# Kernel tuning notes

Measured on AMD Instinct MI355X. Metric: run time of the kernel, lower is better.

## Reference

```python
import jax, jax.numpy as jnp
import numpy as np

BATCH = 32768
HIDDEN = 512
OUT = 2
FUTURE_STEPS = 60


def _lstm_cell(x, h, c, w_ih, w_hh, b_ih, b_hh):
    # PyTorch gate order: i, f, g, o
    g = x @ w_ih.T + h @ w_hh.T + b_ih + b_hh
    i, f, gg, o = jnp.split(g, 4, axis=-1)
    c_new = jax.nn.sigmoid(f) * c + jax.nn.sigmoid(i) * jnp.tanh(gg)
    h_new = jax.nn.sigmoid(o) * jnp.tanh(c_new)
    return h_new, c_new


def setup_inputs() -> dict:
    key = jax.random.key(0)
    ks = jax.random.split(key, 16)
    s = 0.05
    inp = {
        "h": jax.random.normal(ks[0], (BATCH, HIDDEN), jnp.float32),
        "w_init_h": jax.random.normal(ks[1], (HIDDEN, HIDDEN), jnp.float32) * s,
        "b_init_h": jax.random.normal(ks[2], (HIDDEN,), jnp.float32) * s,
        "w_init_c": jax.random.normal(ks[3], (HIDDEN, HIDDEN), jnp.float32) * s,
        "b_init_c": jax.random.normal(ks[4], (HIDDEN,), jnp.float32) * s,
        "w_ih0": jax.random.normal(ks[5], (4 * HIDDEN, OUT), jnp.float32) * s,
        "w_hh0": jax.random.normal(ks[6], (4 * HIDDEN, HIDDEN), jnp.float32) * s,
        "b_ih0": jax.random.normal(ks[7], (4 * HIDDEN,), jnp.float32) * s,
        "b_hh0": jax.random.normal(ks[8], (4 * HIDDEN,), jnp.float32) * s,
        "w_ih1": jax.random.normal(ks[9], (4 * HIDDEN, HIDDEN), jnp.float32) * s,
        "w_hh1": jax.random.normal(ks[10], (4 * HIDDEN, HIDDEN), jnp.float32) * s,
        "b_ih1": jax.random.normal(ks[11], (4 * HIDDEN,), jnp.float32) * s,
        "b_hh1": jax.random.normal(ks[12], (4 * HIDDEN,), jnp.float32) * s,
        "w_out": jax.random.normal(ks[13], (OUT, HIDDEN), jnp.float32) * s,
        "b_out": jax.random.normal(ks[14], (OUT,), jnp.float32) * s,
    }
    return inp


def reference(h, w_init_h, b_init_h, w_init_c, b_init_c,
              w_ih0, w_hh0, b_ih0, b_hh0,
              w_ih1, w_hh1, b_ih1, b_hh1,
              w_out, b_out):
    batch = h.shape[0]
    # same initial (h, c) replicated to both LSTM layers (repeat(2,1,1))
    h0 = h @ w_init_h.T + b_init_h
    c0 = h @ w_init_c.T + b_init_c
    x0 = jnp.zeros((batch, OUT), h.dtype)

    def step(carry, _):
        x, h1, c1, h2, c2 = carry
        h1, c1 = _lstm_cell(x, h1, c1, w_ih0, w_hh0, b_ih0, b_hh0)
        h2, c2 = _lstm_cell(h1, h2, c2, w_ih1, w_hh1, b_ih1, b_hh1)
        pred = h2 @ w_out.T + b_out  # [batch, OUT]
        return (pred, h1, c1, h2, c2), pred

    _, preds = jax.lax.scan(step, (x0, h0, c0, h0, c0), None, length=FUTURE_STEPS)
    return jnp.transpose(preds, (1, 0, 2))  # [batch, future_steps, OUT]
```

## Files before the change

### kernel.cpp

```cpp
#include <hip/hip_runtime.h>

#define HID    512
#define TPB    512
#define NSTEP  60
#define BMI    64

using f32x4 = __attribute__((ext_vector_type(4))) float;
using s16x8 = __attribute__((ext_vector_type(8))) short;

__device__ __forceinline__ unsigned short f2bf(float f) {
    unsigned u = __builtin_bit_cast(unsigned, f);
    u += 0x7fffu + ((u >> 16) & 1u);
    return (unsigned short)(u >> 16);
}
__device__ __forceinline__ float bf2f(unsigned u) {
    return __builtin_bit_cast(float, u << 16);
}
__device__ __forceinline__ float sigm(float x) { return 1.0f / (1.0f + __expf(-x)); }
__device__ __forceinline__ float tanh_(float x) { return 1.0f - 2.0f / (__expf(2.0f * x) + 1.0f); }

__global__ void pack_kernel(const float* __restrict__ w_hh0, const float* __restrict__ w_ih1,
                            const float* __restrict__ w_hh1, const float* __restrict__ w_init_h,
                            const float* __restrict__ w_init_c,
                            const float* __restrict__ b_ih0, const float* __restrict__ b_hh0,
                            const float* __restrict__ b_ih1, const float* __restrict__ b_hh1,
                            unsigned short* __restrict__ PW1, unsigned short* __restrict__ PW2,
                            unsigned short* __restrict__ PI,
                            float* __restrict__ b1, float* __restrict__ b2)
{
    int idx = blockIdx.x * 256 + threadIdx.x;
    if (idx < 1048576) {
        int el = idx & 511, fr = idx >> 9;
        int ks = fr & 15, ct = (fr >> 4) & 7, s = fr >> 7;
        int lane = el >> 3, e = el & 7;
        int cl = ct * 16 + (lane & 15);
        int gcol = (cl >> 5) * 512 + s * 32 + (cl & 31);
        int k = ks * 32 + (lane >> 4) * 8 + e;
        PW1[idx] = f2bf(w_hh0[gcol * 512 + k]);
        return;
    }
    int i2 = idx - 1048576;
    if (i2 >= 0 && i2 < 2097152) {
        int el = i2 & 511, fr = i2 >> 9;
        int ks = fr & 31, ct = (fr >> 5) & 7, s = fr >> 8;
        int lane = el >> 3, e = el & 7;
        int cl = ct * 16 + (lane & 15);
        int gcol = (cl >> 5) * 512 + s * 32 + (cl & 31);
        int kk = (ks & 15) * 32 + (lane >> 4) * 8 + e;
        float v = (ks < 16) ? w_ih1[gcol * 512 + kk] : w_hh1[gcol * 512 + kk];
        PW2[i2] = f2bf(v);
        return;
    }
    int i3 = idx - (1048576 + 2097152);
    if (i3 >= 0 && i3 < 524288) {
        int el = i3 & 511, fr = i3 >> 9;
        int ks = fr & 15, tile = fr >> 4;
        int s = tile >> 5, c = tile & 31;
        int lane = el >> 3, e = el & 7;
        int n = c * 16 + (lane & 15);
        int k = ks * 32 + (lane >> 4) * 8 + e;
        float v = s ? w_init_c[n * 512 + k] : w_init_h[n * 512 + k];
        PI[i3] = f2bf(v);
        return;
    }
    int i4 = idx - (1048576 + 2097152 + 524288);
    if (i4 >= 0 && i4 < 2048) b1[i4] = b_ih0[i4] + b_hh0[i4];
    else if (i4 >= 2048 && i4 < 4096) b2[i4 - 2048] = b_ih1[i4 - 2048] + b_hh1[i4 - 2048];
}

__global__ __launch_bounds__(TPB, 2) void init_kernel(
    const float* __restrict__ hin, const unsigned short* __restrict__ PI,
    const float* __restrict__ b_init_h, const float* __restrict__ b_init_c,
    unsigned short* __restrict__ h1s, unsigned short* __restrict__ h2s,
    unsigned short* __restrict__ c1s, unsigned short* __restrict__ c2s,
    float* __restrict__ xs0, float* __restrict__ xs1)
{
    __shared__ unsigned short bufA[BMI * HID];
    const int tid = threadIdx.x, lane = tid & 63, wave = tid >> 6;
    const int m0 = blockIdx.x * BMI;
    const int l15 = lane & 15, lg = lane >> 4;
    const int swz = (lane & 7) << 4;

    for (int j = 0; j < 16; ++j) {
        int e = tid * 4 + j * 2048;
        int row = e >> 9, col = e & 511;
        float4 v = *(const float4*)(hin + (size_t)(m0 + row) * HID + col);
        ushort4 w;
        w.x = f2bf(v.x); w.y = f2bf(v.y); w.z = f2bf(v.z); w.w = f2bf(v.w);
        int L = (row * 1024 + col * 2) ^ ((row & 7) << 4);
        *(ushort4*)((char*)bufA + L) = w;
    }
    if (tid < 2 * BMI) { xs0[m0 * 2 + tid] = 0.0f; xs1[m0 * 2 + tid] = 0.0f; }
    __syncthreads();

    #pragma unroll 1
    for (int cc = 0; cc < 4; ++cc) {
        int c = wave * 4 + cc;
        int nc = c * 16 + l15;
        f32x4 acc[4][2];
        #pragma unroll
        for (int rt = 0; rt < 4; ++rt)
            #pragma unroll
            for (int s = 0; s < 2; ++s)
                #pragma unroll
                for (int r = 0; r < 4; ++r) acc[rt][s][r] = 0.0f;

        #pragma unroll
        for (int ks = 0; ks < 16; ++ks) {
            s16x8 a[4];
            #pragma unroll
            for (int rt = 0; rt < 4; ++rt) {
                int ao = (rt * 16 + l15) * 1024 + ((ks * 64 + lg * 16) ^ swz);
                a[rt] = *(const s16x8*)((const char*)bufA + ao);
            }
            #pragma unroll
            for (int s = 0; s < 2; ++s) {
                s16x8 b = ((const s16x8*)PI)[((s * 32 + c) * 16 + ks) * 64 + lane];
                #pragma unroll
                for (int rt = 0; rt < 4; ++rt)
                    acc[rt][s] = __builtin_amdgcn_mfma_f32_16x16x32_bf16(a[rt], b, acc[rt][s], 0, 0, 0);
            }
        }
        float bh = b_init_h[nc], bc = b_init_c[nc];
        #pragma unroll
        for (int rt = 0; rt < 4; ++rt)
            #pragma unroll
            for (int r = 0; r < 4; ++r) {
                int m = m0 + rt * 16 + lg * 4 + r;
                float hv = acc[rt][0][r] + bh;
                float cv = acc[rt][1][r] + bc;
                unsigned short hb = f2bf(hv);
                size_t o = (size_t)m * HID + nc;
                h1s[o] = hb; h2s[o] = hb;
                c1s[o] = f2bf(cv); c2s[o] = f2bf(cv);
            }
    }
}

__global__ __launch_bounds__(TPB, 2) void l1_kernel(
    const unsigned short* __restrict__ h1R, unsigned short* __restrict__ h1W,
    unsigned short* __restrict__ c1s,
    const float* __restrict__ xsR, float* __restrict__ xsW,
    float* __restrict__ outp,
    const unsigned short* __restrict__ PW1, const float* __restrict__ b1,
    const float* __restrict__ w_ih0, const float* __restrict__ b_out, int t)
{
    __shared__ __align__(16) unsigned short Ab[32 * HID];
    __shared__ __align__(16) float gl[32 * 128];
    const int tid = threadIdx.x, lane = tid & 63, w = tid >> 6;
    const int b = blockIdx.x;
    const int g = 2 * (b & 7) + (b >> 7);
    const int s = (b >> 3) & 15;
    const int m0 = g * 2048;
    const int l15 = lane & 15, lg = lane >> 4;

    for (int i = tid; i < 2048; i += TPB)
        *(float2*)(xsW + (size_t)(m0 + i) * 2) = make_float2(0.f, 0.f);

    if (t > 0 && s == 0) {
        float a0 = b_out[0], a1 = b_out[1];
        for (int i = tid; i < 2048; i += TPB) {
            float2 v = *(const float2*)(xsR + (size_t)(m0 + i) * 2);
            float* op = outp + (size_t)(m0 + i) * (2 * NSTEP) + (t - 1) * 2;
            op[0] = v.x + a0; op[1] = v.y + a1;
        }
    }

    s16x8 bw[16];
    #pragma unroll
    for (int ks = 0; ks < 16; ++ks)
        bw[ks] = ((const s16x8*)PW1)[((s * 8 + w) * 16 + ks) * 64 + lane];

    const int erow = tid >> 4, ejp = tid & 15;
    float b1v[8], wiA[8], wiB[8];
    #pragma unroll
    for (int q = 0; q < 8; ++q) {
        int dj = q & 1, gq = q >> 1;
        int gcol = gq * 512 + s * 32 + ejp * 2 + dj;
        b1v[q] = b1[gcol];
        wiA[q] = w_ih0[gcol * 2 + 0];
        wiB[q] = w_ih0[gcol * 2 + 1];
    }
    float bo0 = b_out[0], bo1 = b_out[1];

    const char* srcBase = (const char*)h1R + (size_t)m0 * (HID * 2);

    uint4 nv[4];
    #pragma unroll
    for (int p = 0; p < 4; ++p)
        nv[p] = *(const uint4*)(srcBase + p * 8192 + tid * 16);
    #pragma unroll
    for (int p = 0; p < 4; ++p) {
        int off = p * 8192 + tid * 16;
        int row = off >> 10, colb = off & 1023;
        *(uint4*)((char*)Ab + row * 1024 + (colb ^ ((row & 7) << 4))) = nv[p];
    }

    #pragma unroll 1
    for (int ch = 0; ch < 64; ++ch) {
        __syncthreads();

        if (ch < 63) {
            const char* src = srcBase + (size_t)(ch + 1) * 32768;
            #pragma unroll
            for (int p = 0; p < 4; ++p)
                nv[p] = *(const uint4*)(src + p * 8192 + tid * 16);
        }

        f32x4 acc0 = {0.f, 0.f, 0.f, 0.f}, acc1 = {0.f, 0.f, 0.f, 0.f};
        #pragma unroll
        for (int ks = 0; ks < 16; ++ks) {
            int kb = (ks * 64 + lg * 16);
            s16x8 a0 = *(const s16x8*)((const char*)Ab + l15 * 1024 + (kb ^ ((l15 & 7) << 4)));
            s16x8 a1 = *(const s16x8*)((const char*)Ab + (l15 + 16) * 1024 + (kb ^ ((l15 & 7) << 4)));
            acc0 = __builtin_amdgcn_mfma_f32_16x16x32_bf16(a0, bw[ks], acc0, 0, 0, 0);
            acc1 = __builtin_amdgcn_mfma_f32_16x16x32_bf16(a1, bw[ks], acc1, 0, 0, 0);
        }
        {
            int col = w * 16 + l15;
            int base = (col & 31) * 4 + (col >> 5);
            #pragma unroll
            for (int r = 0; r < 4; ++r) {
                gl[(lg * 4 + r) * 128 + base] = acc0[r];
                gl[(16 + lg * 4 + r) * 128 + base] = acc1[r];
            }
        }
        __syncthreads();

        if (ch < 63) {
            #pragma unroll
            for (int p = 0; p < 4; ++p) {
                int off = p * 8192 + tid * 16;
                int row = off >> 10, colb = off & 1023;
                *(uint4*)((char*)Ab + row * 1024 + (colb ^ ((row & 7) << 4))) = nv[p];
            }
        }

        {
            int m = m0 + ch * 32 + erow;
            float x0 = 0.f, x1 = 0.f;
            if (t > 0) {
                float2 xv = *(const float2*)(xsR + (size_t)m * 2);
                x0 = xv.x + bo0; x1 = xv.y + bo1;
            }
            f32x4 ga = *(const f32x4*)(gl + erow * 128 + ejp * 8);
            f32x4 gb = *(const f32x4*)(gl + erow * 128 + ejp * 8 + 4);
            int cix = m * HID + s * 32 + ejp * 2;
            unsigned cp = *(const unsigned*)(c1s + cix);
            float cold0 = bf2f(cp & 0xffffu), cold1 = bf2f(cp >> 16);
            float i0 = sigm(ga[0] + b1v[0] + x0 * wiA[0] + x1 * wiB[0]);
            float f0 = sigm(ga[1] + b1v[2] + x0 * wiA[2] + x1 * wiB[2]);
            float g0 = tanh_(ga[2] + b1v[4] + x0 * wiA[4] + x1 * wiB[4]);
            float o0 = sigm(ga[3] + b1v[6] + x0 * wiA[6] + x1 * wiB[6]);
            float cn0 = f0 * cold0 + i0 * g0;
            float hn0 = o0 * tanh_(cn0);
            float i1 = sigm(gb[0] + b1v[1] + x0 * wiA[1] + x1 * wiB[1]);
            float f1 = sigm(gb[1] + b1v[3] + x0 * wiA[3] + x1 * wiB[3]);
            float g1 = tanh_(gb[2] + b1v[5] + x0 * wiA[5] + x1 * wiB[5]);
            float o1 = sigm(gb[3] + b1v[7] + x0 * wiA[7] + x1 * wiB[7]);
            float cn1 = f1 * cold1 + i1 * g1;
            float hn1 = o1 * tanh_(cn1);
            *(unsigned*)(c1s + cix) = (unsigned)f2bf(cn0) | ((unsigned)f2bf(cn1) << 16);
            *(unsigned*)(h1W + cix) = (unsigned)f2bf(hn0) | ((unsigned)f2bf(hn1) << 16);
        }
    }
}

__global__ __launch_bounds__(TPB, 2) void l2_kernel(
    const unsigned short* __restrict__ h1C, const unsigned short* __restrict__ h2R,
    unsigned short* __restrict__ h2W, unsigned short* __restrict__ c2s,
    float* __restrict__ xsW,
    const unsigned short* __restrict__ PW2, const float* __restrict__ b2,
    const float* __restrict__ w_out)
{
    __shared__ __align__(16) unsigned short Ab[32 * 1024];
    __shared__ __align__(16) float gl[32 * 128];
    const int tid = threadIdx.x, lane = tid & 63, w = tid >> 6;
    const int b = blockIdx.x;
    const int g = 2 * (b & 7) + (b >> 7);
    const int s = (b >> 3) & 15;
    const int m0 = g * 2048;
    const int l15 = lane & 15, lg = lane >> 4;

    s16x8 bw[32];
    #pragma unroll
    for (int ks = 0; ks < 32; ++ks)
        bw[ks] = ((const s16x8*)PW2)[((s * 8 + w) * 32 + ks) * 64 + lane];

    const int erow = tid >> 4, ejp = tid & 15;
    float b2v[8];
    #pragma unroll
    for (int q = 0; q < 8; ++q) {
        int dj = q & 1, gq = q >> 1;
        b2v[q] = b2[gq * 512 + s * 32 + ejp * 2 + dj];
    }
    float woA0 = w_out[s * 32 + ejp * 2], woA1 = w_out[s * 32 + ejp * 2 + 1];
    float woB0 = w_out[512 + s * 32 + ejp * 2], woB1 = w_out[512 + s * 32 + ejp * 2 + 1];

    const char* s1 = (const char*)h1C + (size_t)m0 * 1024;
    const char* s2 = (const char*)h2R + (size_t)m0 * 1024;

    uint4 nv[8];
    #pragma unroll
    for (int p = 0; p < 8; ++p) {
        int off = p * 8192 + tid * 16;
        int row = off >> 11, colb = off & 2047;
        nv[p] = (colb < 1024) ? *(const uint4*)(s1 + row * 1024 + colb)
                              : *(const uint4*)(s2 + row * 1024 + (colb - 1024));
    }
    #pragma unroll
    for (int p = 0; p < 8; ++p) {
        int off = p * 8192 + tid * 16;
        int row = off >> 11, colb = off & 2047;
        *(uint4*)((char*)Ab + row * 2048 + (colb ^ ((row & 7) << 4))) = nv[p];
    }

    #pragma unroll 1
    for (int ch = 0; ch < 64; ++ch) {
        __syncthreads();

        if (ch < 63) {
            #pragma unroll
            for (int p = 0; p < 8; ++p) {
                int off = p * 8192 + tid * 16;
                int row = (ch + 1) * 32 + (off >> 11), colb = off & 2047;
                nv[p] = (colb < 1024) ? *(const uint4*)(s1 + (size_t)row * 1024 + colb)
                                      : *(const uint4*)(s2 + (size_t)row * 1024 + (colb - 1024));
            }
        }

        f32x4 acc0 = {0.f, 0.f, 0.f, 0.f}, acc1 = {0.f, 0.f, 0.f, 0.f};
        #pragma unroll
        for (int ks = 0; ks < 32; ++ks) {
            int kb = (ks * 64 + lg * 16);
            s16x8 a0 = *(const s16x8*)((const char*)Ab + l15 * 2048 + (kb ^ ((l15 & 7) << 4)));
            s16x8 a1 = *(const s16x8*)((const char*)Ab + (l15 + 16) * 2048 + (kb ^ ((l15 & 7) << 4)));
            acc0 = __builtin_amdgcn_mfma_f32_16x16x32_bf16(a0, bw[ks], acc0, 0, 0, 0);
            acc1 = __builtin_amdgcn_mfma_f32_16x16x32_bf16(a1, bw[ks], acc1, 0, 0, 0);
        }
        {
            int col = w * 16 + l15;
            int base = (col & 31) * 4 + (col >> 5);
            #pragma unroll
            for (int r = 0; r < 4; ++r) {
                gl[(lg * 4 + r) * 128 + base] = acc0[r];
                gl[(16 + lg * 4 + r) * 128 + base] = acc1[r];
            }
        }
        __syncthreads();

        if (ch < 63) {
            #pragma unroll
            for (int p = 0; p < 8; ++p) {
                int off = p * 8192 + tid * 16;
                int row = off >> 11, colb = off & 2047;
                *(uint4*)((char*)Ab + row * 2048 + (colb ^ ((row & 7) << 4))) = nv[p];
            }
        }

        {
            int m = m0 + ch * 32 + erow;
            f32x4 ga = *(const f32x4*)(gl + erow * 128 + ejp * 8);
            f32x4 gb = *(const f32x4*)(gl + erow * 128 + ejp * 8 + 4);
            int cix = m * HID + s * 32 + ejp * 2;
            unsigned cp = *(const unsigned*)(c2s + cix);
            float cold0 = bf2f(cp & 0xffffu), cold1 = bf2f(cp >> 16);
            float i0 = sigm(ga[0] + b2v[0]);
            float f0 = sigm(ga[1] + b2v[2]);
            float g0 = tanh_(ga[2] + b2v[4]);
            float o0 = sigm(ga[3] + b2v[6]);
            float cn0 = f0 * cold0 + i0 * g0;
            float hn0 = o0 * tanh_(cn0);
            float i1 = sigm(gb[0] + b2v[1]);
            float f1 = sigm(gb[1] + b2v[3]);
            float g1 = tanh_(gb[2] + b2v[5]);
            float o1 = sigm(gb[3] + b2v[7]);
            float cn1 = f1 * cold1 + i1 * g1;
            float hn1 = o1 * tanh_(cn1);
            *(unsigned*)(c2s + cix) = (unsigned)f2bf(cn0) | ((unsigned)f2bf(cn1) << 16);
            *(unsigned*)(h2W + cix) = (unsigned)f2bf(hn0) | ((unsigned)f2bf(hn1) << 16);
            float p0 = hn0 * woA0 + hn1 * woA1;
            float p1 = hn0 * woB0 + hn1 * woB1;
            #pragma unroll
            for (int d = 1; d < 16; d <<= 1) {
                p0 += __shfl_xor(p0, d, 16);
                p1 += __shfl_xor(p1, d, 16);
            }
            if (ejp == 0) {
                atomicAdd(xsW + (size_t)m * 2, p0);
                atomicAdd(xsW + (size_t)m * 2 + 1, p1);
            }
        }
    }
}

__global__ void tail_kernel(const float* __restrict__ xs0, const float* __restrict__ b_out,
                            float* __restrict__ outp)
{
    int i = blockIdx.x * 256 + threadIdx.x;
    if (i < 65536) {
        int m = i >> 1, j = i & 1;
        outp[(size_t)m * (2 * NSTEP) + (NSTEP - 1) * 2 + j] = xs0[i] + b_out[j];
    }
}

extern "C" void kernel_launch(void* const* d_in, const int* in_sizes, int n_in,
                              void* d_out, int out_size, void* d_ws, size_t ws_size,
                              hipStream_t stream)
{
    (void)in_sizes; (void)n_in; (void)out_size; (void)ws_size;
    const float* h        = (const float*)d_in[0];
    const float* w_init_h = (const float*)d_in[1];
    const float* b_init_h = (const float*)d_in[2];
    const float* w_init_c = (const float*)d_in[3];
    const float* b_init_c = (const float*)d_in[4];
    const float* w_ih0    = (const float*)d_in[5];
    const float* w_hh0    = (const float*)d_in[6];
    const float* b_ih0    = (const float*)d_in[7];
    const float* b_hh0    = (const float*)d_in[8];
    const float* w_ih1    = (const float*)d_in[9];
    const float* w_hh1    = (const float*)d_in[10];
    const float* b_ih1    = (const float*)d_in[11];
    const float* b_hh1    = (const float*)d_in[12];
    const float* w_out    = (const float*)d_in[13];
    const float* b_out    = (const float*)d_in[14];
    float* out = (float*)d_out;

    char* ws = (char*)d_ws;
    unsigned short* h1s[2] = { (unsigned short*)(ws + 0),
                               (unsigned short*)(ws + 33554432) };
    unsigned short* h2s[2] = { (unsigned short*)(ws + 67108864),
                               (unsigned short*)(ws + 100663296) };
    unsigned short* c1s = (unsigned short*)(ws + 134217728);
    unsigned short* c2s = (unsigned short*)(ws + 167772160);
    float* xs[2] = { (float*)(ws + 201326592), (float*)(ws + 201588736) };
    unsigned short* PW1 = (unsigned short*)(ws + 201850880);
    unsigned short* PW2 = (unsigned short*)(ws + 203948032);
    unsigned short* PI  = (unsigned short*)(ws + 208142336);
    float* b1 = (float*)(ws + 209190912);
    float* b2 = (float*)(ws + 209199104);

    pack_kernel<<<14352, 256, 0, stream>>>(w_hh0, w_ih1, w_hh1, w_init_h, w_init_c,
                                           b_ih0, b_hh0, b_ih1, b_hh1, PW1, PW2, PI, b1, b2);
    init_kernel<<<32768 / BMI, TPB, 0, stream>>>(h, PI, b_init_h, b_init_c,
                                                 h1s[1], h2s[1], c1s, c2s, xs[0], xs[1]);
    for (int t = 0; t < NSTEP; ++t) {
        const unsigned short* h1R = h1s[(t + 1) & 1];
        unsigned short* h1W = h1s[t & 1];
        const unsigned short* h2R = h2s[(t + 1) & 1];
        unsigned short* h2W = h2s[t & 1];
        const float* xsR = xs[t & 1];
        float* xsW = xs[(t + 1) & 1];
        l1_kernel<<<256, TPB, 0, stream>>>(h1R, h1W, c1s, xsR, xsW, out, PW1, b1,
                                           w_ih0, b_out, t);
        l2_kernel<<<256, TPB, 0, stream>>>(h1W, h2R, h2W, c2s, xsW, PW2, b2, w_out);
    }
    tail_kernel<<<256, 256, 0, stream>>>(xs[0], b_out, out);
}
```

Before: 39.92 ms.

## Split MFMA work over K across waves and replace output atomics with partial sums

Each wave now computes four 16-column tiles over half (l1) or a quarter (l2) of the K range. Partial gate sums are reduced through shared memory with a permuted layout to avoid bank conflicts. The h tiles are staged in MFMA-fragment order, so reads need no swizzle. The global atomicAdd accumulation of the output projection is replaced by per-slice partial buffers that the next l1 kernel and the tail kernel sum. This aims to cut LDS A-operand traffic per MFMA and remove atomic contention, at the cost of extra shared-memory reductions and barriers.

```diff
diff --git a/kernel.cpp b/kernel.cpp
--- a/kernel.cpp
+++ b/kernel.cpp
@@ -18,6 +18,15 @@
 }
 __device__ __forceinline__ float sigm(float x) { return 1.0f / (1.0f + __expf(-x)); }
 __device__ __forceinline__ float tanh_(float x) { return 1.0f - 2.0f / (__expf(2.0f * x) + 1.0f); }
+
+__device__ __forceinline__ f32x4 deperm(f32x4 q, int lgr) {
+    f32x4 p;
+    if (lgr == 0)      { p[0]=q[0]; p[1]=q[1]; p[2]=q[2]; p[3]=q[3]; }
+    else if (lgr == 1) { p[0]=q[1]; p[1]=q[0]; p[2]=q[3]; p[3]=q[2]; }
+    else if (lgr == 2) { p[0]=q[2]; p[1]=q[3]; p[2]=q[0]; p[3]=q[1]; }
+    else               { p[0]=q[3]; p[1]=q[2]; p[2]=q[1]; p[3]=q[0]; }
+    return p;
+}
 
 __global__ void pack_kernel(const float* __restrict__ w_hh0, const float* __restrict__ w_ih1,
                             const float* __restrict__ w_hh1, const float* __restrict__ w_init_h,
@@ -72,8 +81,7 @@
     const float* __restrict__ hin, const unsigned short* __restrict__ PI,
     const float* __restrict__ b_init_h, const float* __restrict__ b_init_c,
     unsigned short* __restrict__ h1s, unsigned short* __restrict__ h2s,
-    unsigned short* __restrict__ c1s, unsigned short* __restrict__ c2s,
-    float* __restrict__ xs0, float* __restrict__ xs1)
+    unsigned short* __restrict__ c1s, unsigned short* __restrict__ c2s)
 {
     __shared__ unsigned short bufA[BMI * HID];
     const int tid = threadIdx.x, lane = tid & 63, wave = tid >> 6;
@@ -90,7 +98,6 @@
         int L = (row * 1024 + col * 2) ^ ((row & 7) << 4);
         *(ushort4*)((char*)bufA + L) = w;
     }
-    if (tid < 2 * BMI) { xs0[m0 * 2 + tid] = 0.0f; xs1[m0 * 2 + tid] = 0.0f; }
     __syncthreads();
 
     #pragma unroll 1
@@ -139,39 +146,32 @@
 
 __global__ __launch_bounds__(TPB, 2) void l1_kernel(
     const unsigned short* __restrict__ h1R, unsigned short* __restrict__ h1W,
-    unsigned short* __restrict__ c1s,
-    const float* __restrict__ xsR, float* __restrict__ xsW,
-    float* __restrict__ outp,
-    const unsigned short* __restrict__ PW1, const float* __restrict__ b1,
-    const float* __restrict__ w_ih0, const float* __restrict__ b_out, int t)
+    unsigned short* __restrict__ c1s, const float* __restrict__ pp,
+    float* __restrict__ outp, const unsigned short* __restrict__ PW1,
+    const float* __restrict__ b1, const float* __restrict__ w_ih0,
+    const float* __restrict__ b_out, int t)
 {
-    __shared__ __align__(16) unsigned short Ab[32 * HID];
-    __shared__ __align__(16) float gl[32 * 128];
+    __shared__ __align__(16) unsigned short Ab[16384];
+    __shared__ __align__(16) float gl[2][2][2048];
+    __shared__ __align__(16) float xls[5120];
+
     const int tid = threadIdx.x, lane = tid & 63, w = tid >> 6;
     const int b = blockIdx.x;
     const int g = 2 * (b & 7) + (b >> 7);
     const int s = (b >> 3) & 15;
     const int m0 = g * 2048;
     const int l15 = lane & 15, lg = lane >> 4;
-
-    for (int i = tid; i < 2048; i += TPB)
-        *(float2*)(xsW + (size_t)(m0 + i) * 2) = make_float2(0.f, 0.f);
-
-    if (t > 0 && s == 0) {
-        float a0 = b_out[0], a1 = b_out[1];
-        for (int i = tid; i < 2048; i += TPB) {
-            float2 v = *(const float2*)(xsR + (size_t)(m0 + i) * 2);
-            float* op = outp + (size_t)(m0 + i) * (2 * NSTEP) + (t - 1) * 2;
-            op[0] = v.x + a0; op[1] = v.y + a1;
-        }
-    }
-
-    s16x8 bw[16];
-    #pragma unroll
-    for (int ks = 0; ks < 16; ++ks)
-        bw[ks] = ((const s16x8*)PW1)[((s * 8 + w) * 16 + ks) * 64 + lane];
+    const int cg = w & 1, kh = (w >> 1) & 1, rha = w >> 2;
+
+    s16x8 bw[4][8];
+    #pragma unroll
+    for (int j = 0; j < 4; ++j)
+        #pragma unroll
+        for (int ksl = 0; ksl < 8; ++ksl)
+            bw[j][ksl] = ((const s16x8*)PW1)[(((s * 8 + cg * 4 + j) * 16) + kh * 8 + ksl) * 64 + lane];
 
     const int erow = tid >> 4, ejp = tid & 15;
+    const int lgr = w & 3;
     float b1v[8], wiA[8], wiB[8];
     #pragma unroll
     for (int q = 0; q < 8; ++q) {
@@ -183,81 +183,109 @@
     }
     float bo0 = b_out[0], bo1 = b_out[1];
 
-    const char* srcBase = (const char*)h1R + (size_t)m0 * (HID * 2);
+    if (t == 0) {
+        #pragma unroll
+        for (int i = 0; i < 8; ++i) xls[tid * 8 + i] = 0.0f;
+    } else {
+        f32x4 s0 = {0.f,0.f,0.f,0.f}, s1 = {0.f,0.f,0.f,0.f};
+        #pragma unroll 1
+        for (int ss = 0; ss < 16; ++ss) {
+            const float* p = pp + (((size_t)(g * 16 + ss)) << 12) + tid * 8;
+            s0 += *(const f32x4*)p;
+            s1 += *(const f32x4*)(p + 4);
+        }
+        s0[0] += bo0; s0[1] += bo1; s0[2] += bo0; s0[3] += bo1;
+        s1[0] += bo0; s1[1] += bo1; s1[2] += bo0; s1[3] += bo1;
+        *(f32x4*)(xls + tid * 8) = s0;
+        *(f32x4*)(xls + tid * 8 + 4) = s1;
+        if (s == 0) {
+            float* ob = outp + (size_t)(m0 + tid * 4) * (2 * NSTEP) + (t - 1) * 2;
+            *(float2*)(ob)                 = make_float2(s0[0], s0[1]);
+            *(float2*)(ob + 2 * NSTEP)     = make_float2(s0[2], s0[3]);
+            *(float2*)(ob + 4 * NSTEP)     = make_float2(s1[0], s1[1]);
+            *(float2*)(ob + 6 * NSTEP)     = make_float2(s1[2], s1[3]);
+        }
+    }
+
+    const int sl15 = tid & 15, slg = (tid >> 4) & 3, srh = (tid >> 6) & 1, skq = tid >> 7;
+    const int sgrow = srh * 16 + sl15;
+    const int scol  = (tid & 15) * 0;
+    (void)scol;
 
     uint4 nv[4];
     #pragma unroll
+    for (int p = 0; p < 4; ++p) {
+        int ks = p * 4 + skq;
+        nv[p] = *(const uint4*)(h1R + (size_t)(m0 + sgrow) * HID + ks * 32 + slg * 8);
+    }
+    #pragma unroll
     for (int p = 0; p < 4; ++p)
-        nv[p] = *(const uint4*)(srcBase + p * 8192 + tid * 16);
-    #pragma unroll
-    for (int p = 0; p < 4; ++p) {
-        int off = p * 8192 + tid * 16;
-        int row = off >> 10, colb = off & 1023;
-        *(uint4*)((char*)Ab + row * 1024 + (colb ^ ((row & 7) << 4))) = nv[p];
-    }
+        *(uint4*)((char*)Ab + p * 8192 + tid * 16) = nv[p];
 
     #pragma unroll 1
     for (int ch = 0; ch < 64; ++ch) {
         __syncthreads();
 
         if (ch < 63) {
-            const char* src = srcBase + (size_t)(ch + 1) * 32768;
+            #pragma unroll
+            for (int p = 0; p < 4; ++p) {
+                int ks = p * 4 + skq;
+                nv[p] = *(const uint4*)(h1R + (size_t)(m0 + (ch + 1) * 32 + sgrow) * HID + ks * 32 + slg * 8);
+            }
+        }
+
+        f32x4 acc[4];
+        #pragma unroll
+        for (int j = 0; j < 4; ++j) { acc[j][0]=0.f; acc[j][1]=0.f; acc[j][2]=0.f; acc[j][3]=0.f; }
+        #pragma unroll
+        for (int ksl = 0; ksl < 8; ++ksl) {
+            int ks = kh * 8 + ksl;
+            s16x8 a = *(const s16x8*)((const char*)Ab + ks * 2048 + rha * 1024 + lane * 16);
+            #pragma unroll
+            for (int j = 0; j < 4; ++j)
+                acc[j] = __builtin_amdgcn_mfma_f32_16x16x32_bf16(a, bw[j][ksl], acc[j], 0, 0, 0);
+        }
+        #pragma unroll
+        for (int j = 0; j < 4; ++j) {
+            int col = (cg * 4 + j) * 16 + l15;
+            int u = col & 31, gate = col >> 5;
+            float* dst = &gl[kh][u & 1][(u >> 1) * 4 + (gate ^ lg)];
+            #pragma unroll
+            for (int r = 0; r < 4; ++r)
+                dst[(rha * 16 + lg * 4 + r) * 64] = acc[j][r];
+        }
+        __syncthreads();
+
+        if (ch < 63) {
             #pragma unroll
             for (int p = 0; p < 4; ++p)
-                nv[p] = *(const uint4*)(src + p * 8192 + tid * 16);
-        }
-
-        f32x4 acc0 = {0.f, 0.f, 0.f, 0.f}, acc1 = {0.f, 0.f, 0.f, 0.f};
-        #pragma unroll
-        for (int ks = 0; ks < 16; ++ks) {
-            int kb = (ks * 64 + lg * 16);
-            s16x8 a0 = *(const s16x8*)((const char*)Ab + l15 * 1024 + (kb ^ ((l15 & 7) << 4)));
-            s16x8 a1 = *(const s16x8*)((const char*)Ab + (l15 + 16) * 1024 + (kb ^ ((l15 & 7) << 4)));
-            acc0 = __builtin_amdgcn_mfma_f32_16x16x32_bf16(a0, bw[ks], acc0, 0, 0, 0);
-            acc1 = __builtin_amdgcn_mfma_f32_16x16x32_bf16(a1, bw[ks], acc1, 0, 0, 0);
-        }
+                *(uint4*)((char*)Ab + p * 8192 + tid * 16) = nv[p];
+        }
+
         {
-            int col = w * 16 + l15;
-            int base = (col & 31) * 4 + (col >> 5);
-            #pragma unroll
-            for (int r = 0; r < 4; ++r) {
-                gl[(lg * 4 + r) * 128 + base] = acc0[r];
-                gl[(16 + lg * 4 + r) * 128 + base] = acc1[r];
-            }
-        }
-        __syncthreads();
-
-        if (ch < 63) {
-            #pragma unroll
-            for (int p = 0; p < 4; ++p) {
-                int off = p * 8192 + tid * 16;
-                int row = off >> 10, colb = off & 1023;
-                *(uint4*)((char*)Ab + row * 1024 + (colb ^ ((row & 7) << 4))) = nv[p];
-            }
-        }
-
-        {
-            int m = m0 + ch * 32 + erow;
-            float x0 = 0.f, x1 = 0.f;
-            if (t > 0) {
-                float2 xv = *(const float2*)(xsR + (size_t)m * 2);
-                x0 = xv.x + bo0; x1 = xv.y + bo1;
-            }
-            f32x4 ga = *(const f32x4*)(gl + erow * 128 + ejp * 8);
-            f32x4 gb = *(const f32x4*)(gl + erow * 128 + ejp * 8 + 4);
+            int grow = ch * 32 + erow;
+            int m = m0 + grow;
+            float x0 = xls[grow * 2 + 0], x1 = xls[grow * 2 + 1];
+            int gbase = erow * 64 + ejp * 4;
+            f32x4 qa = *(const f32x4*)&gl[0][0][gbase];
+            qa += *(const f32x4*)&gl[1][0][gbase];
+            f32x4 qb = *(const f32x4*)&gl[0][1][gbase];
+            qb += *(const f32x4*)&gl[1][1][gbase];
+            qa = deperm(qa, lgr); qb = deperm(qb, lgr);
+
             int cix = m * HID + s * 32 + ejp * 2;
             unsigned cp = *(const unsigned*)(c1s + cix);
             float cold0 = bf2f(cp & 0xffffu), cold1 = bf2f(cp >> 16);
-            float i0 = sigm(ga[0] + b1v[0] + x0 * wiA[0] + x1 * wiB[0]);
-            float f0 = sigm(ga[1] + b1v[2] + x0 * wiA[2] + x1 * wiB[2]);
-            float g0 = tanh_(ga[2] + b1v[4] + x0 * wiA[4] + x1 * wiB[4]);
-            float o0 = sigm(ga[3] + b1v[6] + x0 * wiA[6] + x1 * wiB[6]);
+            float i0 = sigm(qa[0] + b1v[0] + x0 * wiA[0] + x1 * wiB[0]);
+            float f0 = sigm(qa[1] + b1v[2] + x0 * wiA[2] + x1 * wiB[2]);
+            float g0 = tanh_(qa[2] + b1v[4] + x0 * wiA[4] + x1 * wiB[4]);
+            float o0 = sigm(qa[3] + b1v[6] + x0 * wiA[6] + x1 * wiB[6]);
             float cn0 = f0 * cold0 + i0 * g0;
             float hn0 = o0 * tanh_(cn0);
-            float i1 = sigm(gb[0] + b1v[1] + x0 * wiA[1] + x1 * wiB[1]);
-            float f1 = sigm(gb[1] + b1v[3] + x0 * wiA[3] + x1 * wiB[3]);
-            float g1 = tanh_(gb[2] + b1v[5] + x0 * wiA[5] + x1 * wiB[5]);
-            float o1 = sigm(gb[3] + b1v[7] + x0 * wiA[7] + x1 * wiB[7]);
+            float i1 = sigm(qb[0] + b1v[1] + x0 * wiA[1] + x1 * wiB[1]);
+            float f1 = sigm(qb[1] + b1v[3] + x0 * wiA[3] + x1 * wiB[3]);
+            float g1 = tanh_(qb[2] + b1v[5] + x0 * wiA[5] + x1 * wiB[5]);
+            float o1 = sigm(qb[3] + b1v[7] + x0 * wiA[7] + x1 * wiB[7]);
             float cn1 = f1 * cold1 + i1 * g1;
             float hn1 = o1 * tanh_(cn1);
             *(unsigned*)(c1s + cix) = (unsigned)f2bf(cn0) | ((unsigned)f2bf(cn1) << 16);
@@ -269,25 +297,31 @@
 __global__ __launch_bounds__(TPB, 2) void l2_kernel(
     const unsigned short* __restrict__ h1C, const unsigned short* __restrict__ h2R,
     unsigned short* __restrict__ h2W, unsigned short* __restrict__ c2s,
-    float* __restrict__ xsW,
+    float* __restrict__ pp,
     const unsigned short* __restrict__ PW2, const float* __restrict__ b2,
     const float* __restrict__ w_out)
 {
-    __shared__ __align__(16) unsigned short Ab[32 * 1024];
-    __shared__ __align__(16) float gl[32 * 128];
+    __shared__ __align__(16) unsigned short Ab[32768];
+    __shared__ __align__(16) float gl[2][2][2304];
+
     const int tid = threadIdx.x, lane = tid & 63, w = tid >> 6;
     const int b = blockIdx.x;
     const int g = 2 * (b & 7) + (b >> 7);
     const int s = (b >> 3) & 15;
     const int m0 = g * 2048;
     const int l15 = lane & 15, lg = lane >> 4;
-
-    s16x8 bw[32];
-    #pragma unroll
-    for (int ks = 0; ks < 32; ++ks)
-        bw[ks] = ((const s16x8*)PW2)[((s * 8 + w) * 32 + ks) * 64 + lane];
+    const int cg = w & 1, kq = w >> 1;
+    const int copy = kq >> 1, adder = ((kq & 1) == 0);
+
+    s16x8 bw[4][8];
+    #pragma unroll
+    for (int j = 0; j < 4; ++j)
+        #pragma unroll
+        for (int ksl = 0; ksl < 8; ++ksl)
+            bw[j][ksl] = ((const s16x8*)PW2)[(((s * 8 + cg * 4 + j) * 32) + kq * 8 + ksl) * 64 + lane];
 
     const int erow = tid >> 4, ejp = tid & 15;
+    const int lgr = w & 3;
     float b2v[8];
     #pragma unroll
     for (int q = 0; q < 8; ++q) {
@@ -297,23 +331,20 @@
     float woA0 = w_out[s * 32 + ejp * 2], woA1 = w_out[s * 32 + ejp * 2 + 1];
     float woB0 = w_out[512 + s * 32 + ejp * 2], woB1 = w_out[512 + s * 32 + ejp * 2 + 1];
 
-    const char* s1 = (const char*)h1C + (size_t)m0 * 1024;
-    const char* s2 = (const char*)h2R + (size_t)m0 * 1024;
+    const int sl15 = tid & 15, slg = (tid >> 4) & 3, srh = (tid >> 6) & 1, skq = tid >> 7;
+    const int sgrow = srh * 16 + sl15;
 
     uint4 nv[8];
     #pragma unroll
     for (int p = 0; p < 8; ++p) {
-        int off = p * 8192 + tid * 16;
-        int row = off >> 11, colb = off & 2047;
-        nv[p] = (colb < 1024) ? *(const uint4*)(s1 + row * 1024 + colb)
-                              : *(const uint4*)(s2 + row * 1024 + (colb - 1024));
-    }
-    #pragma unroll
-    for (int p = 0; p < 8; ++p) {
-        int off = p * 8192 + tid * 16;
-        int row = off >> 11, colb = off & 2047;
-        *(uint4*)((char*)Ab + row * 2048 + (colb ^ ((row & 7) << 4))) = nv[p];
-    }
+        int ks = p * 4 + skq;
+        const unsigned short* src = (p < 4) ? h1C : h2R;
+        int kel = (p < 4) ? ks : (ks - 16);
+        nv[p] = *(const uint4*)(src + (size_t)(m0 + sgrow) * HID + kel * 32 + slg * 8);
+    }
+    #pragma unroll
+    for (int p = 0; p < 8; ++p)
+        *(uint4*)((char*)Ab + p * 8192 + tid * 16) = nv[p];
 
     #pragma unroll 1
     for (int ch = 0; ch < 64; ++ch) {
@@ -322,63 +353,92 @@
         if (ch < 63) {
             #pragma unroll
             for (int p = 0; p < 8; ++p) {
-                int off = p * 8192 + tid * 16;
-                int row = (ch + 1) * 32 + (off >> 11), colb = off & 2047;
-                nv[p] = (colb < 1024) ? *(const uint4*)(s1 + (size_t)row * 1024 + colb)
-                                      : *(const uint4*)(s2 + (size_t)row * 1024 + (colb - 1024));
-            }
-        }
-
-        f32x4 acc0 = {0.f, 0.f, 0.f, 0.f}, acc1 = {0.f, 0.f, 0.f, 0.f};
-        #pragma unroll
-        for (int ks = 0; ks < 32; ++ks) {
-            int kb = (ks * 64 + lg * 16);
-            s16x8 a0 = *(const s16x8*)((const char*)Ab + l15 * 2048 + (kb ^ ((l15 & 7) << 4)));
-            s16x8 a1 = *(const s16x8*)((const char*)Ab + (l15 + 16) * 2048 + (kb ^ ((l15 & 7) << 4)));
-            acc0 = __builtin_amdgcn_mfma_f32_16x16x32_bf16(a0, bw[ks], acc0, 0, 0, 0);
-            acc1 = __builtin_amdgcn_mfma_f32_16x16x32_bf16(a1, bw[ks], acc1, 0, 0, 0);
-        }
-        {
-            int col = w * 16 + l15;
-            int base = (col & 31) * 4 + (col >> 5);
-            #pragma unroll
-            for (int r = 0; r < 4; ++r) {
-                gl[(lg * 4 + r) * 128 + base] = acc0[r];
-                gl[(16 + lg * 4 + r) * 128 + base] = acc1[r];
+                int ks = p * 4 + skq;
+                const unsigned short* src = (p < 4) ? h1C : h2R;
+                int kel = (p < 4) ? ks : (ks - 16);
+                nv[p] = *(const uint4*)(src + (size_t)(m0 + (ch + 1) * 32 + sgrow) * HID + kel * 32 + slg * 8);
+            }
+        }
+
+        f32x4 acc[2][4];
+        #pragma unroll
+        for (int rh = 0; rh < 2; ++rh)
+            #pragma unroll
+            for (int j = 0; j < 4; ++j) { acc[rh][j][0]=0.f; acc[rh][j][1]=0.f; acc[rh][j][2]=0.f; acc[rh][j][3]=0.f; }
+        #pragma unroll
+        for (int ksl = 0; ksl < 8; ++ksl) {
+            int ks = kq * 8 + ksl;
+            s16x8 a0 = *(const s16x8*)((const char*)Ab + ks * 2048 + lane * 16);
+            s16x8 a1 = *(const s16x8*)((const char*)Ab + ks * 2048 + 1024 + lane * 16);
+            #pragma unroll
+            for (int j = 0; j < 4; ++j) {
+                acc[0][j] = __builtin_amdgcn_mfma_f32_16x16x32_bf16(a0, bw[j][ksl], acc[0][j], 0, 0, 0);
+                acc[1][j] = __builtin_amdgcn_mfma_f32_16x16x32_bf16(a1, bw[j][ksl], acc[1][j], 0, 0, 0);
+            }
+        }
+
+        if (!adder) {
+            #pragma unroll
+            for (int j = 0; j < 4; ++j) {
+                int col = (cg * 4 + j) * 16 + l15;
+                int u = col & 31, gate = col >> 5;
+                float* dst = &gl[copy][u & 1][(u >> 1) * 4 + (gate ^ lg)];
+                #pragma unroll
+                for (int rh = 0; rh < 2; ++rh)
+                    #pragma unroll
+                    for (int r = 0; r < 4; ++r)
+                        dst[(rh * 16 + lg * 4 + r) * 64] = acc[rh][j][r];
             }
         }
         __syncthreads();
+        if (adder) {
+            #pragma unroll
+            for (int j = 0; j < 4; ++j) {
+                int col = (cg * 4 + j) * 16 + l15;
+                int u = col & 31, gate = col >> 5;
+                float* dst = &gl[copy][u & 1][(u >> 1) * 4 + (gate ^ lg)];
+                #pragma unroll
+                for (int rh = 0; rh < 2; ++rh)
+                    #pragma unroll
+                    for (int r = 0; r < 4; ++r)
+                        dst[(rh * 16 + lg * 4 + r) * 64] += acc[rh][j][r];
+            }
+        }
+        __syncthreads();
 
         if (ch < 63) {
             #pragma unroll
-            for (int p = 0; p < 8; ++p) {
-                int off = p * 8192 + tid * 16;
-                int row = off >> 11, colb = off & 2047;
-                *(uint4*)((char*)Ab + row * 2048 + (colb ^ ((row & 7) << 4))) = nv[p];
-            }
+            for (int p = 0; p < 8; ++p)
+                *(uint4*)((char*)Ab + p * 8192 + tid * 16) = nv[p];
         }
 
         {
             int m = m0 + ch * 32 + erow;
-            f32x4 ga = *(const f32x4*)(gl + erow * 128 + ejp * 8);
-            f32x4 gb = *(const f32x4*)(gl + erow * 128 + ejp * 8 + 4);
+            int gbase = erow * 64 + ejp * 4;
+            f32x4 qa = *(const f32x4*)&gl[0][0][gbase];
+            qa += *(const f32x4*)&gl[1][0][gbase];
+            f32x4 qb = *(const f32x4*)&gl[0][1][gbase];
+            qb += *(const f32x4*)&gl[1][1][gbase];
+            qa = deperm(qa, lgr); qb = deperm(qb, lgr);
+
             int cix = m * HID + s * 32 + ejp * 2;
             unsigned cp = *(const unsigned*)(c2s + cix);
             float cold0 = bf2f(cp & 0xffffu), cold1 = bf2f(cp >> 16);
-            float i0 = sigm(ga[0] + b2v[0]);
-            float f0 = sigm(ga[1] + b2v[2]);
-            float g0 = tanh_(ga[2] + b2v[4]);
-            float o0 = sigm(ga[3] + b2v[6]);
+            float i0 = sigm(qa[0] + b2v[0]);
+            float f0 = sigm(qa[1] + b2v[2]);
+            float g0 = tanh_(qa[2] + b2v[4]);
+            float o0 = sigm(qa[3] + b2v[6]);
             float cn0 = f0 * cold0 + i0 * g0;
             float hn0 = o0 * tanh_(cn0);
-            float i1 = sigm(gb[0] + b2v[1]);
-            float f1 = sigm(gb[1] + b2v[3]);
-            float g1 = tanh_(gb[2] + b2v[5]);
-            float o1 = sigm(gb[3] + b2v[7]);
+            float i1 = sigm(qb[0] + b2v[1]);
+            float f1 = sigm(qb[1] + b2v[3]);
+            float g1 = tanh_(qb[2] + b2v[5]);
+            float o1 = sigm(qb[3] + b2v[7]);
             float cn1 = f1 * cold1 + i1 * g1;
             float hn1 = o1 * tanh_(cn1);
             *(unsigned*)(c2s + cix) = (unsigned)f2bf(cn0) | ((unsigned)f2bf(cn1) << 16);
             *(unsigned*)(h2W + cix) = (unsigned)f2bf(hn0) | ((unsigned)f2bf(hn1) << 16);
+
             float p0 = hn0 * woA0 + hn1 * woA1;
             float p1 = hn0 * woB0 + hn1 * woB1;
             #pragma unroll
@@ -386,21 +446,26 @@
                 p0 += __shfl_xor(p0, d, 16);
                 p1 += __shfl_xor(p1, d, 16);
             }
-            if (ejp == 0) {
-                atomicAdd(xsW + (size_t)m * 2, p0);
-                atomicAdd(xsW + (size_t)m * 2 + 1, p1);
-            }
-        }
-    }
-}
-
-__global__ void tail_kernel(const float* __restrict__ xs0, const float* __restrict__ b_out,
+            if (ejp == 0)
+                *(float2*)(pp + (((size_t)(g * 16 + s)) << 12) + (size_t)(ch * 32 + erow) * 2)
+                    = make_float2(p0, p1);
+        }
+    }
+}
+
+__global__ void tail_kernel(const float* __restrict__ pp, const float* __restrict__ b_out,
                             float* __restrict__ outp)
 {
     int i = blockIdx.x * 256 + threadIdx.x;
     if (i < 65536) {
         int m = i >> 1, j = i & 1;
-        outp[(size_t)m * (2 * NSTEP) + (NSTEP - 1) * 2 + j] = xs0[i] + b_out[j];
+        int g = m >> 11;
+        int idx = (m & 2047) * 2 + j;
+        float sum = b_out[j];
+        #pragma unroll 1
+        for (int s = 0; s < 16; ++s)
+            sum += pp[(((size_t)(g * 16 + s)) << 12) + idx];
+        outp[(size_t)m * (2 * NSTEP) + (NSTEP - 1) * 2 + j] = sum;
     }
 }
 
@@ -433,27 +498,24 @@
                                (unsigned short*)(ws + 100663296) };
     unsigned short* c1s = (unsigned short*)(ws + 134217728);
     unsigned short* c2s = (unsigned short*)(ws + 167772160);
-    float* xs[2] = { (float*)(ws + 201326592), (float*)(ws + 201588736) };
-    unsigned short* PW1 = (unsigned short*)(ws + 201850880);
-    unsigned short* PW2 = (unsigned short*)(ws + 203948032);
-    unsigned short* PI  = (unsigned short*)(ws + 208142336);
-    float* b1 = (float*)(ws + 209190912);
-    float* b2 = (float*)(ws + 209199104);
+    float* pp           = (float*)(ws + 201326592);
+    unsigned short* PW1 = (unsigned short*)(ws + 205520896);
+    unsigned short* PW2 = (unsigned short*)(ws + 207618048);
+    unsigned short* PI  = (unsigned short*)(ws + 211812352);
+    float* b1 = (float*)(ws + 212860928);
+    float* b2 = (float*)(ws + 212869120);
 
     pack_kernel<<<14352, 256, 0, stream>>>(w_hh0, w_ih1, w_hh1, w_init_h, w_init_c,
                                            b_ih0, b_hh0, b_ih1, b_hh1, PW1, PW2, PI, b1, b2);
     init_kernel<<<32768 / BMI, TPB, 0, stream>>>(h, PI, b_init_h, b_init_c,
-                                                 h1s[1], h2s[1], c1s, c2s, xs[0], xs[1]);
+                                                 h1s[1], h2s[1], c1s, c2s);
     for (int t = 0; t < NSTEP; ++t) {
         const unsigned short* h1R = h1s[(t + 1) & 1];
         unsigned short* h1W = h1s[t & 1];
         const unsigned short* h2R = h2s[(t + 1) & 1];
         unsigned short* h2W = h2s[t & 1];
-        const float* xsR = xs[t & 1];
-        float* xsW = xs[(t + 1) & 1];
-        l1_kernel<<<256, TPB, 0, stream>>>(h1R, h1W, c1s, xsR, xsW, out, PW1, b1,
-                                           w_ih0, b_out, t);
-        l2_kernel<<<256, TPB, 0, stream>>>(h1W, h2R, h2W, c2s, xsW, PW2, b2, w_out);
-    }
-    tail_kernel<<<256, 256, 0, stream>>>(xs[0], b_out, out);
-}
+        l1_kernel<<<256, TPB, 0, stream>>>(h1R, h1W, c1s, pp, out, PW1, b1, w_ih0, b_out, t);
+        l2_kernel<<<256, TPB, 0, stream>>>(h1W, h2R, h2W, c2s, pp, PW2, b2, w_out);
+    }
+    tail_kernel<<<256, 256, 0, stream>>>(pp, b_out, out);
+}
```

After: 38.76 ms. -2.9%, faster.
